# Performance work log

Measured on AMD Instinct MI355X. Metric: run time of the kernel, lower is better.

## Reference

```python
import jax, jax.numpy as jnp
import numpy as np

EMBED_DIM = 1024
ATTN_DIM = 1024
BATCH = 4
SEQ = 2048


def setup_inputs() -> dict:
    key = jax.random.key(0)
    k1, k2, k3, k4 = jax.random.split(key, 4)
    embedded = jax.random.normal(k1, (BATCH, SEQ, EMBED_DIM), dtype=jnp.float32)
    # torch Linear weights have shape [out_features, in_features]
    scale = 1.0 / np.sqrt(EMBED_DIM)
    W_K = jax.random.uniform(k2, (ATTN_DIM, EMBED_DIM), dtype=jnp.float32, minval=-scale, maxval=scale)
    W_Q = jax.random.uniform(k3, (ATTN_DIM, EMBED_DIM), dtype=jnp.float32, minval=-scale, maxval=scale)
    W_V = jax.random.uniform(k4, (ATTN_DIM, EMBED_DIM), dtype=jnp.float32, minval=-scale, maxval=scale)
    return {"embedded": embedded, "W_K": W_K, "W_Q": W_Q, "W_V": W_V}


def reference(embedded, W_K, W_Q, W_V):
    # embedded: [B, L, E]; W_*: [A, E] (torch Linear layout, applied as x @ W.T)
    L = embedded.shape[1]
    A = W_K.shape[0]
    K = jnp.einsum('ble,ae->bla', embedded, W_K)
    Q = jnp.einsum('ble,ae->bla', embedded, W_Q)
    V = jnp.einsum('ble,ae->bla', embedded, W_V)
    att = jnp.einsum('bqa,bka->bqk', Q, K) / jnp.sqrt(jnp.float32(A))  # [B, L, L]
    causal = jnp.tril(jnp.ones((L, L), dtype=bool))  # lower-triangular mask
    att = jnp.where(causal, att, -jnp.inf)
    att = jax.nn.softmax(att, axis=-1)
    return jnp.einsum('bqk,bka->bqa', att, V)
```

## Files before the change

kernel.cpp:

```cpp
#include <hip/hip_runtime.h>
#include <hip/hip_bf16.h>
#include <stdint.h>

#define BATCH 4
#define SEQ   2048
#define EMB   1024
#define ADIM  1024

typedef __attribute__((ext_vector_type(8))) short  short8;
typedef __attribute__((ext_vector_type(4))) float  float4v;

static __device__ __forceinline__ unsigned short f2bf(float f) {
    unsigned int u = __float_as_uint(f);
    u += 0x7FFFu + ((u >> 16) & 1u);
    return (unsigned short)(u >> 16);
}

static __device__ __forceinline__ uint2 pack4(float4v v) {
    uint2 r;
    r.x = (unsigned)f2bf(v.x) | ((unsigned)f2bf(v.y) << 16);
    r.y = (unsigned)f2bf(v.z) | ((unsigned)f2bf(v.w) << 16);
    return r;
}

static __device__ __forceinline__ void gload16(const void* g, void* l) {
    __builtin_amdgcn_global_load_lds(
        (const __attribute__((address_space(1))) void*)g,
        (__attribute__((address_space(3))) void*)l, 16, 0, 0);
}

__global__ __launch_bounds__(256) void prep_kernel(
    const float* __restrict__ X,  const float* __restrict__ Wv,
    const float* __restrict__ Wq, const float* __restrict__ Wk,
    unsigned short* __restrict__ Xb, unsigned short* __restrict__ Wvb,
    unsigned short* __restrict__ WqT, unsigned short* __restrict__ WkT,
    float* __restrict__ rowsum)
{
    __shared__ unsigned short T[64][72];
    const int bI = blockIdx.x;
    if (bI < 4608) {
        const float* src; unsigned short* dst; int off;
        if (bI < 4096) { src = X;  dst = Xb;  off = bI; }
        else           { src = Wv; dst = Wvb; off = bI - 4096; }
        const int i = (off * 256 + threadIdx.x) * 8;
        float4v a = *(const float4v*)(src + i);
        float4v b = *(const float4v*)(src + i + 4);
        uint2 pa = pack4(a), pb = pack4(b);
        uint4 o; o.x = pa.x; o.y = pa.y; o.z = pb.x; o.w = pb.y;
        *(uint4*)(dst + i) = o;
        return;
    }
    if (bI < 4616) {
        const int i = ((bI - 4616) * 256 + threadIdx.x) * 4;
        *(float4v*)(rowsum + i) = float4v{0.f, 0.f, 0.f, 0.f};
        return;
    }
    const int z    = (bI - 4616) >> 8;
    const int tile = (bI - 4616) & 255;
    const int ti = tile >> 4;
    const int tj = tile & 15;
    const float* W = z ? Wk : Wq;
    unsigned short* WT = z ? WkT : WqT;
    const int t  = threadIdx.x;
    const int r  = t >> 2;
    const int c  = (t & 3) << 4;

    const float* src = W + (size_t)(ti * 64 + r) * EMB + tj * 64 + c;
    #pragma unroll
    for (int u = 0; u < 4; ++u) {
        float4v v = *(const float4v*)(src + 4 * u);
        uint2 p = pack4(v);
        *(uint2*)&T[r][c + 4 * u] = p;
    }
    __syncthreads();
    unsigned short tmp[16];
    #pragma unroll
    for (int u = 0; u < 16; ++u) tmp[u] = T[c + u][r];
    unsigned short* dst = WT + (size_t)(tj * 64 + r) * EMB + ti * 64 + c;
    *(uint4*)(dst)     = *(uint4*)&tmp[0];
    *(uint4*)(dst + 8) = *(uint4*)&tmp[8];
}

static __device__ __forceinline__ void gemm_core(
    const unsigned short* __restrict__ A, const unsigned short* __restrict__ B,
    int lda, int ldb, int m0, int n0, int kend,
    unsigned short* As, unsigned short* Bs, float4v acc[4][4])
{
    const int tid  = threadIdx.x;
    const int r    = tid >> 2;
    const int c8   = (tid & 3) << 3;
    const int lane = tid & 63;
    const int wave = tid >> 6;
    const int quad = lane >> 4;
    const int l16  = lane & 15;
    const int wm   = (wave >> 1) << 6;
    const int wn   = (wave & 1) << 6;

    const unsigned short* Ag = A + (size_t)(m0 + r) * lda + c8;
    const unsigned short* Bg = B + (size_t)(n0 + r) * ldb + c8;
    unsigned short* Al = As + tid * 8;
    unsigned short* Bl = Bs + tid * 8;
    const int niter = kend >> 5;

    #define ISSUE(k0, st) do { \
        unsigned short* al_ = Al + (st) * 4096; \
        unsigned short* bl_ = Bl + (st) * 4096; \
        gload16(Ag + (k0),                    al_); \
        gload16(Ag + (k0) + (size_t)64 * lda, al_ + 2048); \
        gload16(Bg + (k0),                    bl_); \
        gload16(Bg + (k0) + (size_t)64 * ldb, bl_ + 2048); \
    } while (0)

    ISSUE(0, 0);
    ISSUE(32, 1);

    int ci = 0, ii = 2;
    for (int it = 0; it < niter; ++it) {
        const int knext = (it + 2 < niter) ? ((it + 2) << 5) : 0;
        ISSUE(knext, ii);
        asm volatile("s_waitcnt vmcnt(8)" ::: "memory");
        asm volatile("s_barrier" ::: "memory");

        const unsigned short* Ah = As + ci * 4096;
        const unsigned short* Bh = Bs + ci * 4096;
        short8 af[4], bfr[4];
        #pragma unroll
        for (int i = 0; i < 4; ++i)
            af[i] = *(const short8*)&Ah[(wm + 16 * i + l16) * 32 + quad * 8];
        #pragma unroll
        for (int j = 0; j < 4; ++j)
            bfr[j] = *(const short8*)&Bh[(wn + 16 * j + l16) * 32 + quad * 8];
        #pragma unroll
        for (int i = 0; i < 4; ++i)
            #pragma unroll
            for (int j = 0; j < 4; ++j)
                acc[i][j] = __builtin_amdgcn_mfma_f32_16x16x32_bf16(af[i], bfr[j], acc[i][j], 0, 0, 0);

        asm volatile("s_barrier" ::: "memory");
        ci = (ci == 2) ? 0 : ci + 1;
        ii = (ii == 2) ? 0 : ii + 1;
    }
    asm volatile("s_waitcnt vmcnt(0)" ::: "memory");
    #undef ISSUE
}

#define DECL_TILE_IDX() \
    const int lane = threadIdx.x & 63; \
    const int wave = threadIdx.x >> 6; \
    const int quad = lane >> 4; \
    const int l16  = lane & 15; \
    const int wm   = (wave >> 1) << 6; \
    const int wn   = (wave & 1) << 6;

__global__ __launch_bounds__(256, 3) void m_kernel(
    const unsigned short* __restrict__ WkT, const unsigned short* __restrict__ WqT,
    unsigned short* __restrict__ Mt)
{
    __shared__ __align__(16) unsigned short As[3 * 128 * 32];
    __shared__ __align__(16) unsigned short Bs[3 * 128 * 32];
    const int m0 = (blockIdx.x >> 3) << 7;
    const int n0 = (blockIdx.x & 7) << 7;

    float4v acc[4][4];
    #pragma unroll
    for (int i = 0; i < 4; ++i)
        #pragma unroll
        for (int j = 0; j < 4; ++j)
            acc[i][j] = float4v{0.f, 0.f, 0.f, 0.f};

    gemm_core(WkT, WqT, EMB, EMB, m0, n0, EMB, As, Bs, acc);

    DECL_TILE_IDX();
    const float scale = 0.03125f;
    #pragma unroll
    for (int i = 0; i < 4; ++i)
        #pragma unroll
        for (int j = 0; j < 4; ++j)
            #pragma unroll
            for (int rr = 0; rr < 4; ++rr) {
                const int row = m0 + wm + 16 * i + quad * 4 + rr;
                const int col = n0 + wn + 16 * j + l16;
                Mt[(size_t)row * EMB + col] = f2bf(acc[i][j][rr] * scale);
            }
}

__global__ __launch_bounds__(256, 2) void qv_kernel(
    const unsigned short* __restrict__ Xb, const unsigned short* __restrict__ Mt,
    const unsigned short* __restrict__ Wvb,
    unsigned short* __restrict__ Qpb, unsigned short* __restrict__ Vtb)
{
    __shared__ __align__(16) unsigned short LDS[3 * 4096 + 3 * 8192];
    unsigned short* As = LDS;
    unsigned short* Bs = LDS + 3 * 4096;
    const int idx   = blockIdx.x;
    const int mlow  = idx & 7;
    const int n0    = ((idx >> 3) & 3) << 8;
    const int mhigh = (idx >> 5) & 7;
    const int z     = idx >> 8;
    const int m0    = ((mhigh << 3) | mlow) << 7;
    const unsigned short* B = (z == 0) ? Mt : Wvb;

    const int tid  = threadIdx.x;
    const int r    = tid >> 2;
    const int c8   = (tid & 3) << 3;
    const int lane = tid & 63;
    const int wave = tid >> 6;
    const int quad = lane >> 4;
    const int l16  = lane & 15;
    const int wm   = (wave >> 1) << 6;
    const int wn   = (wave & 1) << 7;

    float4v acc[4][8];
    #pragma unroll
    for (int i = 0; i < 4; ++i)
        #pragma unroll
        for (int j = 0; j < 8; ++j)
            acc[i][j] = float4v{0.f, 0.f, 0.f, 0.f};

    const unsigned short* Ag = Xb + (size_t)(m0 + r) * EMB + c8;
    const unsigned short* Bg = B  + (size_t)(n0 + r) * EMB + c8;
    unsigned short* Al = As + tid * 8;
    unsigned short* Bl = Bs + tid * 8;

    #define ISSUE_W(k0, st) do { \
        unsigned short* al_ = Al + (st) * 4096; \
        unsigned short* bl_ = Bl + (st) * 8192; \
        gload16(Ag + (k0),                     al_); \
        gload16(Ag + (k0) + (size_t)64  * EMB, al_ + 2048); \
        gload16(Bg + (k0),                     bl_); \
        gload16(Bg + (k0) + (size_t)64  * EMB, bl_ + 2048); \
        gload16(Bg + (k0) + (size_t)128 * EMB, bl_ + 4096); \
        gload16(Bg + (k0) + (size_t)192 * EMB, bl_ + 6144); \
    } while (0)

    ISSUE_W(0, 0);
    ISSUE_W(32, 1);

    int ci = 0, ii = 2;
    for (int it = 0; it < 32; ++it) {
        const int knext = (it + 2 < 32) ? ((it + 2) << 5) : 0;
        ISSUE_W(knext, ii);
        asm volatile("s_waitcnt vmcnt(12)" ::: "memory");
        asm volatile("s_barrier" ::: "memory");

        const unsigned short* Ah = As + ci * 4096;
        const unsigned short* Bh = Bs + ci * 8192;
        short8 af[4], bfr[8];
        #pragma unroll
        for (int i = 0; i < 4; ++i)
            af[i] = *(const short8*)&Ah[(wm + 16 * i + l16) * 32 + quad * 8];
        #pragma unroll
        for (int j = 0; j < 8; ++j)
            bfr[j] = *(const short8*)&Bh[(wn + 16 * j + l16) * 32 + quad * 8];
        #pragma unroll
        for (int i = 0; i < 4; ++i)
            #pragma unroll
            for (int j = 0; j < 8; ++j)
                acc[i][j] = __builtin_amdgcn_mfma_f32_16x16x32_bf16(af[i], bfr[j], acc[i][j], 0, 0, 0);

        asm volatile("s_barrier" ::: "memory");
        ci = (ci == 2) ? 0 : ci + 1;
        ii = (ii == 2) ? 0 : ii + 1;
    }
    asm volatile("s_waitcnt vmcnt(0)" ::: "memory");
    #undef ISSUE_W

    if (z == 0) {
        #pragma unroll
        for (int i = 0; i < 4; ++i)
            #pragma unroll
            for (int j = 0; j < 8; ++j)
                #pragma unroll
                for (int rr = 0; rr < 4; ++rr) {
                    const int row = m0 + wm + 16 * i + quad * 4 + rr;
                    const int col = n0 + wn + 16 * j + l16;
                    Qpb[(size_t)row * ADIM + col] = f2bf(acc[i][j][rr]);
                }
    } else {
        __syncthreads();
        unsigned short* T = LDS;
        #pragma unroll
        for (int i = 0; i < 4; ++i)
            #pragma unroll
            for (int j = 0; j < 8; ++j) {
                const int qrow = wm + 16 * i + quad * 4;
                const int acol = wn + 16 * j + l16;
                uint2 w;
                w.x = (unsigned)f2bf(acc[i][j][0]) | ((unsigned)f2bf(acc[i][j][1]) << 16);
                w.y = (unsigned)f2bf(acc[i][j][2]) | ((unsigned)f2bf(acc[i][j][3]) << 16);
                *(uint2*)&T[acol * 136 + qrow] = w;
            }
        __syncthreads();
        const int bb = m0 >> 11;
        const int l0 = m0 & (SEQ - 1);
        unsigned short* dst = Vtb + (((size_t)(bb * ADIM + n0 + tid)) << 11) + l0;
        #pragma unroll
        for (int u = 0; u < 16; ++u)
            *(uint4*)(dst + u * 8) = *(const uint4*)&T[tid * 136 + u * 8];
    }
}

__global__ __launch_bounds__(256, 3) void s_kernel(
    const unsigned short* __restrict__ Qpb, const unsigned short* __restrict__ Xb,
    unsigned short* __restrict__ E, float* __restrict__ rowsum)
{
    const int idx = blockIdx.x;
    const int b   = idx & 3;
    const int tri = idx >> 2;
    int qt = 0;
    while (((qt + 1) * (qt + 2)) / 2 <= tri) ++qt;
    const int kt = tri - (qt * (qt + 1)) / 2;
    const int q0 = qt << 7;
    const int k0 = kt << 7;

    __shared__ __align__(16) unsigned short As[3 * 128 * 32];
    __shared__ __align__(16) unsigned short Bs[3 * 128 * 32];

    float4v acc[4][4];
    #pragma unroll
    for (int i = 0; i < 4; ++i)
        #pragma unroll
        for (int j = 0; j < 4; ++j)
            acc[i][j] = float4v{0.f, 0.f, 0.f, 0.f};

    gemm_core(Qpb + (size_t)b * SEQ * ADIM, Xb + (size_t)b * SEQ * EMB,
              ADIM, EMB, q0, k0, EMB, As, Bs, acc);

    unsigned short* Eb = E + (size_t)b * SEQ * SEQ;
    float* rsb = rowsum + (size_t)b * SEQ;
    DECL_TILE_IDX();
    #pragma unroll
    for (int i = 0; i < 4; ++i)
        #pragma unroll
        for (int rr = 0; rr < 4; ++rr) {
            const int row = q0 + wm + 16 * i + quad * 4 + rr;
            float s = 0.f;
            #pragma unroll
            for (int j = 0; j < 4; ++j) {
                const int col = k0 + wn + 16 * j + l16;
                float e = (col <= row) ? __expf(acc[i][j][rr]) : 0.f;
                s += e;
                Eb[(size_t)row * SEQ + col] = f2bf(e);
            }
            s += __shfl_xor(s, 1);
            s += __shfl_xor(s, 2);
            s += __shfl_xor(s, 4);
            s += __shfl_xor(s, 8);
            if (l16 == 0) atomicAdd(&rsb[row], s);
        }
}

__global__ __launch_bounds__(256, 3) void pv_kernel(
    const unsigned short* __restrict__ E, const unsigned short* __restrict__ Vtb,
    const float* __restrict__ rowsum, float* __restrict__ out)
{
    const int idx = blockIdx.x;
    const int t   = (idx < 256) ? (15 - (idx >> 5)) : ((idx - 256) >> 5);
    const int rem = idx & 31;
    const int b   = rem >> 3;
    const int a0  = (rem & 7) << 7;
    const int q0  = t << 7;

    __shared__ __align__(16) unsigned short As[3 * 128 * 32];
    __shared__ __align__(16) unsigned short Bs[3 * 128 * 32];

    float4v acc[4][4];
    #pragma unroll
    for (int i = 0; i < 4; ++i)
        #pragma unroll
        for (int j = 0; j < 4; ++j)
            acc[i][j] = float4v{0.f, 0.f, 0.f, 0.f};

    gemm_core(E + (size_t)b * SEQ * SEQ, Vtb + (size_t)b * ADIM * SEQ,
              SEQ, SEQ, q0, a0, q0 + 128, As, Bs, acc);

    float* ob = out + (size_t)b * SEQ * ADIM;
    const float* rsb = rowsum + (size_t)b * SEQ;
    DECL_TILE_IDX();
    #pragma unroll
    for (int i = 0; i < 4; ++i)
        #pragma unroll
        for (int rr = 0; rr < 4; ++rr) {
            const int row = q0 + wm + 16 * i + quad * 4 + rr;
            const float inv = 1.0f / rsb[row];
            #pragma unroll
            for (int j = 0; j < 4; ++j) {
                const int col = a0 + wn + 16 * j + l16;
                ob[(size_t)row * ADIM + col] = acc[i][j][rr] * inv;
            }
        }
}

extern "C" void kernel_launch(void* const* d_in, const int* in_sizes, int n_in,
                              void* d_out, int out_size, void* d_ws, size_t ws_size,
                              hipStream_t stream)
{
    const float* X  = (const float*)d_in[0];
    const float* Wk = (const float*)d_in[1];
    const float* Wq = (const float*)d_in[2];
    const float* Wv = (const float*)d_in[3];
    float* out = (float*)d_out;

    const size_t MB = 1024 * 1024;
    char* ws = (char*)d_ws;
    unsigned short* Xb  = (unsigned short*)(ws);
    unsigned short* Wvb = (unsigned short*)(ws + 16 * MB);
    unsigned short* WqT = (unsigned short*)(ws + 18 * MB);
    unsigned short* WkT = (unsigned short*)(ws + 20 * MB);
    unsigned short* Mt  = (unsigned short*)(ws + 22 * MB);
    unsigned short* Qpb = (unsigned short*)(ws + 24 * MB);
    unsigned short* E   = (unsigned short*)(ws + 40 * MB);
    unsigned short* Vtb = (unsigned short*)(ws + 72 * MB);
    float*          rowsum = (float*)(ws + 88 * MB);

    hipLaunchKernelGGL(prep_kernel, dim3(5128), dim3(256), 0, stream,
                       X, Wv, Wq, Wk, Xb, Wvb, WqT, WkT, rowsum);
    hipLaunchKernelGGL(m_kernel, dim3(64), dim3(256), 0, stream, WkT, WqT, Mt);
    hipLaunchKernelGGL(qv_kernel, dim3(512), dim3(256), 0, stream,
                       Xb, Mt, Wvb, Qpb, Vtb);
    hipLaunchKernelGGL(s_kernel, dim3(4 * 136), dim3(256), 0, stream, Qpb, Xb, E, rowsum);
    hipLaunchKernelGGL(pv_kernel, dim3(512), dim3(256), 0, stream, E, Vtb, rowsum, out);
}
```

Measured before the change: 228.2 us.

## Deepen GEMM pipeline to four stages and retile qv kernel to 128x128

The shared GEMM core moves from a three-stage to a four-stage LDS prefetch ring with a wait count adjusted to match. Occupancy hints drop from three to two blocks per CU to make room for the larger LDS. The qv kernel stops using its own 128x256 loop and calls the shared 128x128 gemm_core over twice as many blocks, with a reworked V-transpose store. The rowsum zeroing index, which was negative before and wrote out of bounds, is also corrected. The aim is more memory-latency hiding and better load balance, at the cost of lower occupancy and more reloads of the A tile.

```diff
diff --git a/kernel.cpp b/kernel.cpp
--- a/kernel.cpp
+++ b/kernel.cpp
@@ -51,7 +51,7 @@
         return;
     }
     if (bI < 4616) {
-        const int i = ((bI - 4616) * 256 + threadIdx.x) * 4;
+        const int i = ((bI - 4608) * 256 + threadIdx.x) * 4;
         *(float4v*)(rowsum + i) = float4v{0.f, 0.f, 0.f, 0.f};
         return;
     }
@@ -113,12 +113,13 @@
 
     ISSUE(0, 0);
     ISSUE(32, 1);
-
-    int ci = 0, ii = 2;
+    ISSUE(64, 2);
+
+    int ci = 0, ii = 3;
     for (int it = 0; it < niter; ++it) {
-        const int knext = (it + 2 < niter) ? ((it + 2) << 5) : 0;
+        const int knext = (it + 3 < niter) ? ((it + 3) << 5) : 0;
         ISSUE(knext, ii);
-        asm volatile("s_waitcnt vmcnt(8)" ::: "memory");
+        asm volatile("s_waitcnt vmcnt(12)" ::: "memory");
         asm volatile("s_barrier" ::: "memory");
 
         const unsigned short* Ah = As + ci * 4096;
@@ -137,8 +138,8 @@
                 acc[i][j] = __builtin_amdgcn_mfma_f32_16x16x32_bf16(af[i], bfr[j], acc[i][j], 0, 0, 0);
 
         asm volatile("s_barrier" ::: "memory");
-        ci = (ci == 2) ? 0 : ci + 1;
-        ii = (ii == 2) ? 0 : ii + 1;
+        ci = (ci + 1) & 3;
+        ii = (ii + 1) & 3;
     }
     asm volatile("s_waitcnt vmcnt(0)" ::: "memory");
     #undef ISSUE
@@ -152,12 +153,12 @@
     const int wm   = (wave >> 1) << 6; \
     const int wn   = (wave & 1) << 6;
 
-__global__ __launch_bounds__(256, 3) void m_kernel(
+__global__ __launch_bounds__(256, 2) void m_kernel(
     const unsigned short* __restrict__ WkT, const unsigned short* __restrict__ WqT,
     unsigned short* __restrict__ Mt)
 {
-    __shared__ __align__(16) unsigned short As[3 * 128 * 32];
-    __shared__ __align__(16) unsigned short Bs[3 * 128 * 32];
+    __shared__ __align__(16) unsigned short As[4 * 128 * 32];
+    __shared__ __align__(16) unsigned short Bs[4 * 128 * 32];
     const int m0 = (blockIdx.x >> 3) << 7;
     const int n0 = (blockIdx.x & 7) << 7;
 
@@ -189,87 +190,32 @@
     const unsigned short* __restrict__ Wvb,
     unsigned short* __restrict__ Qpb, unsigned short* __restrict__ Vtb)
 {
-    __shared__ __align__(16) unsigned short LDS[3 * 4096 + 3 * 8192];
+    __shared__ __align__(16) unsigned short LDS[2 * 4 * 128 * 32];
     unsigned short* As = LDS;
-    unsigned short* Bs = LDS + 3 * 4096;
+    unsigned short* Bs = LDS + 4 * 128 * 32;
     const int idx   = blockIdx.x;
     const int mlow  = idx & 7;
-    const int n0    = ((idx >> 3) & 3) << 8;
-    const int mhigh = (idx >> 5) & 7;
-    const int z     = idx >> 8;
+    const int n0    = ((idx >> 3) & 7) << 7;
+    const int mhigh = (idx >> 6) & 7;
+    const int z     = idx >> 9;
     const int m0    = ((mhigh << 3) | mlow) << 7;
     const unsigned short* B = (z == 0) ? Mt : Wvb;
 
-    const int tid  = threadIdx.x;
-    const int r    = tid >> 2;
-    const int c8   = (tid & 3) << 3;
-    const int lane = tid & 63;
-    const int wave = tid >> 6;
-    const int quad = lane >> 4;
-    const int l16  = lane & 15;
-    const int wm   = (wave >> 1) << 6;
-    const int wn   = (wave & 1) << 7;
-
-    float4v acc[4][8];
-    #pragma unroll
-    for (int i = 0; i < 4; ++i)
-        #pragma unroll
-        for (int j = 0; j < 8; ++j)
+    float4v acc[4][4];
+    #pragma unroll
+    for (int i = 0; i < 4; ++i)
+        #pragma unroll
+        for (int j = 0; j < 4; ++j)
             acc[i][j] = float4v{0.f, 0.f, 0.f, 0.f};
 
-    const unsigned short* Ag = Xb + (size_t)(m0 + r) * EMB + c8;
-    const unsigned short* Bg = B  + (size_t)(n0 + r) * EMB + c8;
-    unsigned short* Al = As + tid * 8;
-    unsigned short* Bl = Bs + tid * 8;
-
-    #define ISSUE_W(k0, st) do { \
-        unsigned short* al_ = Al + (st) * 4096; \
-        unsigned short* bl_ = Bl + (st) * 8192; \
-        gload16(Ag + (k0),                     al_); \
-        gload16(Ag + (k0) + (size_t)64  * EMB, al_ + 2048); \
-        gload16(Bg + (k0),                     bl_); \
-        gload16(Bg + (k0) + (size_t)64  * EMB, bl_ + 2048); \
-        gload16(Bg + (k0) + (size_t)128 * EMB, bl_ + 4096); \
-        gload16(Bg + (k0) + (size_t)192 * EMB, bl_ + 6144); \
-    } while (0)
-
-    ISSUE_W(0, 0);
-    ISSUE_W(32, 1);
-
-    int ci = 0, ii = 2;
-    for (int it = 0; it < 32; ++it) {
-        const int knext = (it + 2 < 32) ? ((it + 2) << 5) : 0;
-        ISSUE_W(knext, ii);
-        asm volatile("s_waitcnt vmcnt(12)" ::: "memory");
-        asm volatile("s_barrier" ::: "memory");
-
-        const unsigned short* Ah = As + ci * 4096;
-        const unsigned short* Bh = Bs + ci * 8192;
-        short8 af[4], bfr[8];
+    gemm_core(Xb, B, EMB, EMB, m0, n0, EMB, As, Bs, acc);
+
+    DECL_TILE_IDX();
+    if (z == 0) {
         #pragma unroll
         for (int i = 0; i < 4; ++i)
-            af[i] = *(const short8*)&Ah[(wm + 16 * i + l16) * 32 + quad * 8];
-        #pragma unroll
-        for (int j = 0; j < 8; ++j)
-            bfr[j] = *(const short8*)&Bh[(wn + 16 * j + l16) * 32 + quad * 8];
-        #pragma unroll
-        for (int i = 0; i < 4; ++i)
-            #pragma unroll
-            for (int j = 0; j < 8; ++j)
-                acc[i][j] = __builtin_amdgcn_mfma_f32_16x16x32_bf16(af[i], bfr[j], acc[i][j], 0, 0, 0);
-
-        asm volatile("s_barrier" ::: "memory");
-        ci = (ci == 2) ? 0 : ci + 1;
-        ii = (ii == 2) ? 0 : ii + 1;
-    }
-    asm volatile("s_waitcnt vmcnt(0)" ::: "memory");
-    #undef ISSUE_W
-
-    if (z == 0) {
-        #pragma unroll
-        for (int i = 0; i < 4; ++i)
-            #pragma unroll
-            for (int j = 0; j < 8; ++j)
+            #pragma unroll
+            for (int j = 0; j < 4; ++j)
                 #pragma unroll
                 for (int rr = 0; rr < 4; ++rr) {
                     const int row = m0 + wm + 16 * i + quad * 4 + rr;
@@ -282,7 +228,7 @@
         #pragma unroll
         for (int i = 0; i < 4; ++i)
             #pragma unroll
-            for (int j = 0; j < 8; ++j) {
+            for (int j = 0; j < 4; ++j) {
                 const int qrow = wm + 16 * i + quad * 4;
                 const int acol = wn + 16 * j + l16;
                 uint2 w;
@@ -291,16 +237,19 @@
                 *(uint2*)&T[acol * 136 + qrow] = w;
             }
         __syncthreads();
-        const int bb = m0 >> 11;
-        const int l0 = m0 & (SEQ - 1);
-        unsigned short* dst = Vtb + (((size_t)(bb * ADIM + n0 + tid)) << 11) + l0;
-        #pragma unroll
-        for (int u = 0; u < 16; ++u)
-            *(uint4*)(dst + u * 8) = *(const uint4*)&T[tid * 136 + u * 8];
-    }
-}
-
-__global__ __launch_bounds__(256, 3) void s_kernel(
+        const int tid = threadIdx.x;
+        const int bb  = m0 >> 11;
+        const int l0  = m0 & (SEQ - 1);
+        const int acol = tid >> 1;
+        const int qh   = (tid & 1) << 6;
+        unsigned short* dst = Vtb + (((size_t)(bb * ADIM + n0 + acol)) << 11) + l0 + qh;
+        #pragma unroll
+        for (int u = 0; u < 8; ++u)
+            *(uint4*)(dst + u * 8) = *(const uint4*)&T[acol * 136 + qh + u * 8];
+    }
+}
+
+__global__ __launch_bounds__(256, 2) void s_kernel(
     const unsigned short* __restrict__ Qpb, const unsigned short* __restrict__ Xb,
     unsigned short* __restrict__ E, float* __restrict__ rowsum)
 {
@@ -313,8 +262,8 @@
     const int q0 = qt << 7;
     const int k0 = kt << 7;
 
-    __shared__ __align__(16) unsigned short As[3 * 128 * 32];
-    __shared__ __align__(16) unsigned short Bs[3 * 128 * 32];
+    __shared__ __align__(16) unsigned short As[4 * 128 * 32];
+    __shared__ __align__(16) unsigned short Bs[4 * 128 * 32];
 
     float4v acc[4][4];
     #pragma unroll
@@ -350,7 +299,7 @@
         }
 }
 
-__global__ __launch_bounds__(256, 3) void pv_kernel(
+__global__ __launch_bounds__(256, 2) void pv_kernel(
     const unsigned short* __restrict__ E, const unsigned short* __restrict__ Vtb,
     const float* __restrict__ rowsum, float* __restrict__ out)
 {
@@ -361,8 +310,8 @@
     const int a0  = (rem & 7) << 7;
     const int q0  = t << 7;
 
-    __shared__ __align__(16) unsigned short As[3 * 128 * 32];
-    __shared__ __align__(16) unsigned short Bs[3 * 128 * 32];
+    __shared__ __align__(16) unsigned short As[4 * 128 * 32];
+    __shared__ __align__(16) unsigned short Bs[4 * 128 * 32];
 
     float4v acc[4][4];
     #pragma unroll
@@ -416,7 +365,7 @@
     hipLaunchKernelGGL(prep_kernel, dim3(5128), dim3(256), 0, stream,
                        X, Wv, Wq, Wk, Xb, Wvb, WqT, WkT, rowsum);
     hipLaunchKernelGGL(m_kernel, dim3(64), dim3(256), 0, stream, WkT, WqT, Mt);
-    hipLaunchKernelGGL(qv_kernel, dim3(512), dim3(256), 0, stream,
+    hipLaunchKernelGGL(qv_kernel, dim3(1024), dim3(256), 0, stream,
                        Xb, Mt, Wvb, Qpb, Vtb);
     hipLaunchKernelGGL(s_kernel, dim3(4 * 136), dim3(256), 0, stream, Qpb, Xb, E, rowsum);
     hipLaunchKernelGGL(pv_kernel, dim3(512), dim3(256), 0, stream, E, Vtb, rowsum, out);
```

After: 246.1 us. 1.08x slower.

## Enlarge qv_kernel tiles to 256x256 and fix rowsum zeroing index

Applied to the files above, without the earlier changes.

The fused Q/V projection GEMM moves from 128x256 to 256x256 output tiles per block. Each wave now holds an 8x8 grid of MFMA accumulators, the grid halves to 256 blocks, and a swizzled block index groups blocks by M tile. This raises arithmetic intensity per LDS and global load and cuts total global traffic, at the cost of one block per CU, heavy register use, and the V transpose now running in two LDS passes. It also fixes the rowsum zeroing offset, which previously computed a negative index and did not clear the buffer.

```diff
diff --git a/kernel.cpp b/kernel.cpp
--- a/kernel.cpp
+++ b/kernel.cpp
@@ -51,7 +51,7 @@
         return;
     }
     if (bI < 4616) {
-        const int i = ((bI - 4616) * 256 + threadIdx.x) * 4;
+        const int i = ((bI - 4608) * 256 + threadIdx.x) * 4;
         *(float4v*)(rowsum + i) = float4v{0.f, 0.f, 0.f, 0.f};
         return;
     }
@@ -184,21 +184,23 @@
             }
 }
 
-__global__ __launch_bounds__(256, 2) void qv_kernel(
+__global__ __launch_bounds__(256, 1) void qv_kernel(
     const unsigned short* __restrict__ Xb, const unsigned short* __restrict__ Mt,
     const unsigned short* __restrict__ Wvb,
     unsigned short* __restrict__ Qpb, unsigned short* __restrict__ Vtb)
 {
-    __shared__ __align__(16) unsigned short LDS[3 * 4096 + 3 * 8192];
+    __shared__ __align__(16) unsigned short LDS[49152];
     unsigned short* As = LDS;
-    unsigned short* Bs = LDS + 3 * 4096;
-    const int idx   = blockIdx.x;
-    const int mlow  = idx & 7;
-    const int n0    = ((idx >> 3) & 3) << 8;
-    const int mhigh = (idx >> 5) & 7;
-    const int z     = idx >> 8;
-    const int m0    = ((mhigh << 3) | mlow) << 7;
-    const unsigned short* B = (z == 0) ? Mt : Wvb;
+    unsigned short* Bs = LDS + 24576;
+
+    const int idx  = blockIdx.x;
+    const int swz  = (idx & 7) * 32 + (idx >> 3);
+    const int mt   = swz >> 3;
+    const int slot = swz & 7;
+    const int z    = slot >> 2;
+    const int n0   = (slot & 3) << 8;
+    const int m0   = mt << 8;
+    const unsigned short* B = z ? Wvb : Mt;
 
     const int tid  = threadIdx.x;
     const int r    = tid >> 2;
@@ -207,12 +209,12 @@
     const int wave = tid >> 6;
     const int quad = lane >> 4;
     const int l16  = lane & 15;
-    const int wm   = (wave >> 1) << 6;
+    const int wm   = (wave >> 1) << 7;
     const int wn   = (wave & 1) << 7;
 
-    float4v acc[4][8];
-    #pragma unroll
-    for (int i = 0; i < 4; ++i)
+    float4v acc[8][8];
+    #pragma unroll
+    for (int i = 0; i < 8; ++i)
         #pragma unroll
         for (int j = 0; j < 8; ++j)
             acc[i][j] = float4v{0.f, 0.f, 0.f, 0.f};
@@ -222,38 +224,40 @@
     unsigned short* Al = As + tid * 8;
     unsigned short* Bl = Bs + tid * 8;
 
-    #define ISSUE_W(k0, st) do { \
-        unsigned short* al_ = Al + (st) * 4096; \
+    #define ISSUE_Q(k0, st) do { \
+        unsigned short* al_ = Al + (st) * 8192; \
         unsigned short* bl_ = Bl + (st) * 8192; \
         gload16(Ag + (k0),                     al_); \
         gload16(Ag + (k0) + (size_t)64  * EMB, al_ + 2048); \
+        gload16(Ag + (k0) + (size_t)128 * EMB, al_ + 4096); \
+        gload16(Ag + (k0) + (size_t)192 * EMB, al_ + 6144); \
         gload16(Bg + (k0),                     bl_); \
         gload16(Bg + (k0) + (size_t)64  * EMB, bl_ + 2048); \
         gload16(Bg + (k0) + (size_t)128 * EMB, bl_ + 4096); \
         gload16(Bg + (k0) + (size_t)192 * EMB, bl_ + 6144); \
     } while (0)
 
-    ISSUE_W(0, 0);
-    ISSUE_W(32, 1);
+    ISSUE_Q(0, 0);
+    ISSUE_Q(32, 1);
 
     int ci = 0, ii = 2;
     for (int it = 0; it < 32; ++it) {
         const int knext = (it + 2 < 32) ? ((it + 2) << 5) : 0;
-        ISSUE_W(knext, ii);
-        asm volatile("s_waitcnt vmcnt(12)" ::: "memory");
+        ISSUE_Q(knext, ii);
+        asm volatile("s_waitcnt vmcnt(16)" ::: "memory");
         asm volatile("s_barrier" ::: "memory");
 
-        const unsigned short* Ah = As + ci * 4096;
+        const unsigned short* Ah = As + ci * 8192;
         const unsigned short* Bh = Bs + ci * 8192;
-        short8 af[4], bfr[8];
-        #pragma unroll
-        for (int i = 0; i < 4; ++i)
+        short8 af[8], bfr[8];
+        #pragma unroll
+        for (int i = 0; i < 8; ++i)
             af[i] = *(const short8*)&Ah[(wm + 16 * i + l16) * 32 + quad * 8];
         #pragma unroll
         for (int j = 0; j < 8; ++j)
             bfr[j] = *(const short8*)&Bh[(wn + 16 * j + l16) * 32 + quad * 8];
         #pragma unroll
-        for (int i = 0; i < 4; ++i)
+        for (int i = 0; i < 8; ++i)
             #pragma unroll
             for (int j = 0; j < 8; ++j)
                 acc[i][j] = __builtin_amdgcn_mfma_f32_16x16x32_bf16(af[i], bfr[j], acc[i][j], 0, 0, 0);
@@ -263,11 +267,11 @@
         ii = (ii == 2) ? 0 : ii + 1;
     }
     asm volatile("s_waitcnt vmcnt(0)" ::: "memory");
-    #undef ISSUE_W
+    #undef ISSUE_Q
 
     if (z == 0) {
         #pragma unroll
-        for (int i = 0; i < 4; ++i)
+        for (int i = 0; i < 8; ++i)
             #pragma unroll
             for (int j = 0; j < 8; ++j)
                 #pragma unroll
@@ -277,26 +281,30 @@
                     Qpb[(size_t)row * ADIM + col] = f2bf(acc[i][j][rr]);
                 }
     } else {
-        __syncthreads();
-        unsigned short* T = LDS;
-        #pragma unroll
-        for (int i = 0; i < 4; ++i)
-            #pragma unroll
-            for (int j = 0; j < 8; ++j) {
-                const int qrow = wm + 16 * i + quad * 4;
-                const int acol = wn + 16 * j + l16;
-                uint2 w;
-                w.x = (unsigned)f2bf(acc[i][j][0]) | ((unsigned)f2bf(acc[i][j][1]) << 16);
-                w.y = (unsigned)f2bf(acc[i][j][2]) | ((unsigned)f2bf(acc[i][j][3]) << 16);
-                *(uint2*)&T[acol * 136 + qrow] = w;
-            }
-        __syncthreads();
         const int bb = m0 >> 11;
         const int l0 = m0 & (SEQ - 1);
-        unsigned short* dst = Vtb + (((size_t)(bb * ADIM + n0 + tid)) << 11) + l0;
-        #pragma unroll
-        for (int u = 0; u < 16; ++u)
-            *(uint4*)(dst + u * 8) = *(const uint4*)&T[tid * 136 + u * 8];
+        #pragma unroll
+        for (int h = 0; h < 2; ++h) {
+            __syncthreads();
+            if ((wm >> 7) == h) {
+                #pragma unroll
+                for (int i = 0; i < 8; ++i)
+                    #pragma unroll
+                    for (int j = 0; j < 8; ++j) {
+                        const int qrow = 16 * i + quad * 4;
+                        const int acol = wn + 16 * j + l16;
+                        uint2 w;
+                        w.x = (unsigned)f2bf(acc[i][j][0]) | ((unsigned)f2bf(acc[i][j][1]) << 16);
+                        w.y = (unsigned)f2bf(acc[i][j][2]) | ((unsigned)f2bf(acc[i][j][3]) << 16);
+                        *(uint2*)&LDS[acol * 136 + qrow] = w;
+                    }
+            }
+            __syncthreads();
+            unsigned short* dst = Vtb + (((size_t)(bb * ADIM + n0 + tid)) << 11) + l0 + h * 128;
+            #pragma unroll
+            for (int u = 0; u < 16; ++u)
+                *(uint4*)(dst + u * 8) = *(const uint4*)&LDS[tid * 136 + u * 8];
+        }
     }
 }
 
@@ -416,7 +424,7 @@
     hipLaunchKernelGGL(prep_kernel, dim3(5128), dim3(256), 0, stream,
                        X, Wv, Wq, Wk, Xb, Wvb, WqT, WkT, rowsum);
     hipLaunchKernelGGL(m_kernel, dim3(64), dim3(256), 0, stream, WkT, WqT, Mt);
-    hipLaunchKernelGGL(qv_kernel, dim3(512), dim3(256), 0, stream,
+    hipLaunchKernelGGL(qv_kernel, dim3(256), dim3(256), 0, stream,
                        Xb, Mt, Wvb, Qpb, Vtb);
     hipLaunchKernelGGL(s_kernel, dim3(4 * 136), dim3(256), 0, stream, Qpb, Xb, E, rowsum);
     hipLaunchKernelGGL(pv_kernel, dim3(512), dim3(256), 0, stream, E, Vtb, rowsum, out);
```

New measurement: 240.9 us. 5.6% more time.

## Split-K the weight product and load-balance causal tiles with paired scheduling

Applied to the files above, without the earlier changes.

The M = Wk^T·Wq GEMM is split four ways along K into fp32 partials, which a new reduce kernel sums and converts to bf16, so 256 blocks run instead of 64. The PV kernel splits long causal rows into two K-halves that accumulate into a pre-zeroed output with atomics. The S and QV kernels are re-indexed to pair short and long q-tiles per group for better balance. It also fixes the rowsum zeroing offset. Costs include an extra launch, fp32 partial traffic, atomics on the output, and zeroing half the output in prep.

```diff
diff --git a/kernel.cpp b/kernel.cpp
--- a/kernel.cpp
+++ b/kernel.cpp
@@ -34,7 +34,7 @@
     const float* __restrict__ Wq, const float* __restrict__ Wk,
     unsigned short* __restrict__ Xb, unsigned short* __restrict__ Wvb,
     unsigned short* __restrict__ WqT, unsigned short* __restrict__ WkT,
-    float* __restrict__ rowsum)
+    float* __restrict__ rowsum, float* __restrict__ out)
 {
     __shared__ unsigned short T[64][72];
     const int bI = blockIdx.x;
@@ -51,8 +51,17 @@
         return;
     }
     if (bI < 4616) {
-        const int i = ((bI - 4616) * 256 + threadIdx.x) * 4;
+        const int i = ((bI - 4608) * 256 + threadIdx.x) * 4;
         *(float4v*)(rowsum + i) = float4v{0.f, 0.f, 0.f, 0.f};
+        return;
+    }
+    if (bI >= 5128) {
+        const int o   = bI - 5128;
+        const int b   = o >> 10;
+        const int blk = o & 1023;
+        float* dst = out + ((size_t)(b * 2048 + 1024) * 1024)
+                         + (size_t)blk * 1024 + threadIdx.x * 4;
+        *(float4v*)dst = float4v{0.f, 0.f, 0.f, 0.f};
         return;
     }
     const int z    = (bI - 4616) >> 8;
@@ -83,7 +92,7 @@
 
 static __device__ __forceinline__ void gemm_core(
     const unsigned short* __restrict__ A, const unsigned short* __restrict__ B,
-    int lda, int ldb, int m0, int n0, int kend,
+    int lda, int ldb, int m0, int n0, int klen,
     unsigned short* As, unsigned short* Bs, float4v acc[4][4])
 {
     const int tid  = threadIdx.x;
@@ -100,7 +109,7 @@
     const unsigned short* Bg = B + (size_t)(n0 + r) * ldb + c8;
     unsigned short* Al = As + tid * 8;
     unsigned short* Bl = Bs + tid * 8;
-    const int niter = kend >> 5;
+    const int niter = klen >> 5;
 
     #define ISSUE(k0, st) do { \
         unsigned short* al_ = Al + (st) * 4096; \
@@ -154,12 +163,15 @@
 
 __global__ __launch_bounds__(256, 3) void m_kernel(
     const unsigned short* __restrict__ WkT, const unsigned short* __restrict__ WqT,
-    unsigned short* __restrict__ Mt)
+    float* __restrict__ Mtf)
 {
     __shared__ __align__(16) unsigned short As[3 * 128 * 32];
     __shared__ __align__(16) unsigned short Bs[3 * 128 * 32];
-    const int m0 = (blockIdx.x >> 3) << 7;
-    const int n0 = (blockIdx.x & 7) << 7;
+    const int idx = blockIdx.x;
+    const int kc  = idx >> 6;
+    const int t   = idx & 63;
+    const int m0  = (t >> 3) << 7;
+    const int n0  = (t & 7) << 7;
 
     float4v acc[4][4];
     #pragma unroll
@@ -168,10 +180,10 @@
         for (int j = 0; j < 4; ++j)
             acc[i][j] = float4v{0.f, 0.f, 0.f, 0.f};
 
-    gemm_core(WkT, WqT, EMB, EMB, m0, n0, EMB, As, Bs, acc);
-
+    gemm_core(WkT + kc * 256, WqT + kc * 256, EMB, EMB, m0, n0, 256, As, Bs, acc);
+
+    float* dst = Mtf + (size_t)kc * 1024 * 1024;
     DECL_TILE_IDX();
-    const float scale = 0.03125f;
     #pragma unroll
     for (int i = 0; i < 4; ++i)
         #pragma unroll
@@ -180,8 +192,25 @@
             for (int rr = 0; rr < 4; ++rr) {
                 const int row = m0 + wm + 16 * i + quad * 4 + rr;
                 const int col = n0 + wn + 16 * j + l16;
-                Mt[(size_t)row * EMB + col] = f2bf(acc[i][j][rr] * scale);
+                dst[(size_t)row * EMB + col] = acc[i][j][rr];
             }
+}
+
+__global__ __launch_bounds__(256) void mc_kernel(
+    const float* __restrict__ Mtf, unsigned short* __restrict__ Mt)
+{
+    const int base = (blockIdx.x * 256 + threadIdx.x) * 16;
+    #pragma unroll
+    for (int u = 0; u < 4; ++u) {
+        const int i = base + u * 4;
+        float4v s = *(const float4v*)(Mtf + i);
+        s = s + *(const float4v*)(Mtf + 1048576 + i);
+        s = s + *(const float4v*)(Mtf + 2097152 + i);
+        s = s + *(const float4v*)(Mtf + 3145728 + i);
+        s = s * 0.03125f;
+        uint2 p = pack4(s);
+        *(uint2*)(Mt + i) = p;
+    }
 }
 
 __global__ __launch_bounds__(256, 2) void qv_kernel(
@@ -192,12 +221,16 @@
     __shared__ __align__(16) unsigned short LDS[3 * 4096 + 3 * 8192];
     unsigned short* As = LDS;
     unsigned short* Bs = LDS + 3 * 4096;
-    const int idx   = blockIdx.x;
-    const int mlow  = idx & 7;
-    const int n0    = ((idx >> 3) & 3) << 8;
-    const int mhigh = (idx >> 5) & 7;
-    const int z     = idx >> 8;
-    const int m0    = ((mhigh << 3) | mlow) << 7;
+    const int idx = blockIdx.x;
+    const int x   = idx & 7;
+    const int j   = idx >> 3;
+    const int sl  = j & 7;
+    const int g   = j >> 3;
+    const int z   = sl >> 2;
+    const int n0  = (sl & 3) << 8;
+    const int b   = g & 3;
+    const int qt  = (g >> 2) ? (15 - x) : x;
+    const int m0  = (b * 16 + qt) << 7;
     const unsigned short* B = (z == 0) ? Mt : Wvb;
 
     const int tid  = threadIdx.x;
@@ -214,8 +247,8 @@
     #pragma unroll
     for (int i = 0; i < 4; ++i)
         #pragma unroll
-        for (int j = 0; j < 8; ++j)
-            acc[i][j] = float4v{0.f, 0.f, 0.f, 0.f};
+        for (int jj = 0; jj < 8; ++jj)
+            acc[i][jj] = float4v{0.f, 0.f, 0.f, 0.f};
 
     const unsigned short* Ag = Xb + (size_t)(m0 + r) * EMB + c8;
     const unsigned short* Bg = B  + (size_t)(n0 + r) * EMB + c8;
@@ -250,13 +283,13 @@
         for (int i = 0; i < 4; ++i)
             af[i] = *(const short8*)&Ah[(wm + 16 * i + l16) * 32 + quad * 8];
         #pragma unroll
-        for (int j = 0; j < 8; ++j)
-            bfr[j] = *(const short8*)&Bh[(wn + 16 * j + l16) * 32 + quad * 8];
-        #pragma unroll
-        for (int i = 0; i < 4; ++i)
-            #pragma unroll
-            for (int j = 0; j < 8; ++j)
-                acc[i][j] = __builtin_amdgcn_mfma_f32_16x16x32_bf16(af[i], bfr[j], acc[i][j], 0, 0, 0);
+        for (int jj = 0; jj < 8; ++jj)
+            bfr[jj] = *(const short8*)&Bh[(wn + 16 * jj + l16) * 32 + quad * 8];
+        #pragma unroll
+        for (int i = 0; i < 4; ++i)
+            #pragma unroll
+            for (int jj = 0; jj < 8; ++jj)
+                acc[i][jj] = __builtin_amdgcn_mfma_f32_16x16x32_bf16(af[i], bfr[jj], acc[i][jj], 0, 0, 0);
 
         asm volatile("s_barrier" ::: "memory");
         ci = (ci == 2) ? 0 : ci + 1;
@@ -269,12 +302,12 @@
         #pragma unroll
         for (int i = 0; i < 4; ++i)
             #pragma unroll
-            for (int j = 0; j < 8; ++j)
+            for (int jj = 0; jj < 8; ++jj)
                 #pragma unroll
                 for (int rr = 0; rr < 4; ++rr) {
                     const int row = m0 + wm + 16 * i + quad * 4 + rr;
-                    const int col = n0 + wn + 16 * j + l16;
-                    Qpb[(size_t)row * ADIM + col] = f2bf(acc[i][j][rr]);
+                    const int col = n0 + wn + 16 * jj + l16;
+                    Qpb[(size_t)row * ADIM + col] = f2bf(acc[i][jj][rr]);
                 }
     } else {
         __syncthreads();
@@ -282,12 +315,12 @@
         #pragma unroll
         for (int i = 0; i < 4; ++i)
             #pragma unroll
-            for (int j = 0; j < 8; ++j) {
+            for (int jj = 0; jj < 8; ++jj) {
                 const int qrow = wm + 16 * i + quad * 4;
-                const int acol = wn + 16 * j + l16;
+                const int acol = wn + 16 * jj + l16;
                 uint2 w;
-                w.x = (unsigned)f2bf(acc[i][j][0]) | ((unsigned)f2bf(acc[i][j][1]) << 16);
-                w.y = (unsigned)f2bf(acc[i][j][2]) | ((unsigned)f2bf(acc[i][j][3]) << 16);
+                w.x = (unsigned)f2bf(acc[i][jj][0]) | ((unsigned)f2bf(acc[i][jj][1]) << 16);
+                w.y = (unsigned)f2bf(acc[i][jj][2]) | ((unsigned)f2bf(acc[i][jj][3]) << 16);
                 *(uint2*)&T[acol * 136 + qrow] = w;
             }
         __syncthreads();
@@ -305,13 +338,14 @@
     unsigned short* __restrict__ E, float* __restrict__ rowsum)
 {
     const int idx = blockIdx.x;
-    const int b   = idx & 3;
-    const int tri = idx >> 2;
-    int qt = 0;
-    while (((qt + 1) * (qt + 2)) / 2 <= tri) ++qt;
-    const int kt = tri - (qt * (qt + 1)) / 2;
-    const int q0 = qt << 7;
-    const int k0 = kt << 7;
+    const int x   = idx & 7;
+    const int j   = idx >> 3;
+    const int b   = j / 17;
+    const int u   = j - b * 17;
+    const int qt  = (u <= x) ? x : 15 - x;
+    const int kt  = (u <= x) ? u : u - (x + 1);
+    const int q0  = qt << 7;
+    const int k0  = kt << 7;
 
     __shared__ __align__(16) unsigned short As[3 * 128 * 32];
     __shared__ __align__(16) unsigned short Bs[3 * 128 * 32];
@@ -320,8 +354,8 @@
     #pragma unroll
     for (int i = 0; i < 4; ++i)
         #pragma unroll
-        for (int j = 0; j < 4; ++j)
-            acc[i][j] = float4v{0.f, 0.f, 0.f, 0.f};
+        for (int jj = 0; jj < 4; ++jj)
+            acc[i][jj] = float4v{0.f, 0.f, 0.f, 0.f};
 
     gemm_core(Qpb + (size_t)b * SEQ * ADIM, Xb + (size_t)b * SEQ * EMB,
               ADIM, EMB, q0, k0, EMB, As, Bs, acc);
@@ -336,9 +370,9 @@
             const int row = q0 + wm + 16 * i + quad * 4 + rr;
             float s = 0.f;
             #pragma unroll
-            for (int j = 0; j < 4; ++j) {
-                const int col = k0 + wn + 16 * j + l16;
-                float e = (col <= row) ? __expf(acc[i][j][rr]) : 0.f;
+            for (int jj = 0; jj < 4; ++jj) {
+                const int col = k0 + wn + 16 * jj + l16;
+                float e = (col <= row) ? __expf(acc[i][jj][rr]) : 0.f;
                 s += e;
                 Eb[(size_t)row * SEQ + col] = f2bf(e);
             }
@@ -354,12 +388,19 @@
     const unsigned short* __restrict__ E, const unsigned short* __restrict__ Vtb,
     const float* __restrict__ rowsum, float* __restrict__ out)
 {
-    const int idx = blockIdx.x;
-    const int t   = (idx < 256) ? (15 - (idx >> 5)) : ((idx - 256) >> 5);
-    const int rem = idx & 31;
-    const int b   = rem >> 3;
-    const int a0  = (rem & 7) << 7;
-    const int q0  = t << 7;
+    const int idx  = blockIdx.x;
+    const int x    = idx & 7;
+    const int j    = idx >> 3;
+    const int slot = j >> 5;
+    const int c    = j & 31;
+    const int b    = c >> 3;
+    const int a0   = (c & 7) << 7;
+
+    int qt, kbeg, klen, dual;
+    if (slot == 0)      { qt = x;      kbeg = 0;    klen = (x + 1) << 7; dual = 0; }
+    else if (slot == 1) { qt = 15 - x; kbeg = 0;    klen = 1024;         dual = 1; }
+    else                { qt = 15 - x; kbeg = 1024; klen = (8 - x) << 7; dual = 1; }
+    const int q0 = qt << 7;
 
     __shared__ __align__(16) unsigned short As[3 * 128 * 32];
     __shared__ __align__(16) unsigned short Bs[3 * 128 * 32];
@@ -368,27 +409,42 @@
     #pragma unroll
     for (int i = 0; i < 4; ++i)
         #pragma unroll
-        for (int j = 0; j < 4; ++j)
-            acc[i][j] = float4v{0.f, 0.f, 0.f, 0.f};
-
-    gemm_core(E + (size_t)b * SEQ * SEQ, Vtb + (size_t)b * ADIM * SEQ,
-              SEQ, SEQ, q0, a0, q0 + 128, As, Bs, acc);
+        for (int jj = 0; jj < 4; ++jj)
+            acc[i][jj] = float4v{0.f, 0.f, 0.f, 0.f};
+
+    gemm_core(E + (size_t)b * SEQ * SEQ + kbeg, Vtb + (size_t)b * ADIM * SEQ + kbeg,
+              SEQ, SEQ, q0, a0, klen, As, Bs, acc);
 
     float* ob = out + (size_t)b * SEQ * ADIM;
     const float* rsb = rowsum + (size_t)b * SEQ;
     DECL_TILE_IDX();
-    #pragma unroll
-    for (int i = 0; i < 4; ++i)
-        #pragma unroll
-        for (int rr = 0; rr < 4; ++rr) {
-            const int row = q0 + wm + 16 * i + quad * 4 + rr;
-            const float inv = 1.0f / rsb[row];
-            #pragma unroll
-            for (int j = 0; j < 4; ++j) {
-                const int col = a0 + wn + 16 * j + l16;
-                ob[(size_t)row * ADIM + col] = acc[i][j][rr] * inv;
+    if (!dual) {
+        #pragma unroll
+        for (int i = 0; i < 4; ++i)
+            #pragma unroll
+            for (int rr = 0; rr < 4; ++rr) {
+                const int row = q0 + wm + 16 * i + quad * 4 + rr;
+                const float inv = 1.0f / rsb[row];
+                #pragma unroll
+                for (int jj = 0; jj < 4; ++jj) {
+                    const int col = a0 + wn + 16 * jj + l16;
+                    ob[(size_t)row * ADIM + col] = acc[i][jj][rr] * inv;
+                }
             }
-        }
+    } else {
+        #pragma unroll
+        for (int i = 0; i < 4; ++i)
+            #pragma unroll
+            for (int rr = 0; rr < 4; ++rr) {
+                const int row = q0 + wm + 16 * i + quad * 4 + rr;
+                const float inv = 1.0f / rsb[row];
+                #pragma unroll
+                for (int jj = 0; jj < 4; ++jj) {
+                    const int col = a0 + wn + 16 * jj + l16;
+                    atomicAdd(&ob[(size_t)row * ADIM + col], acc[i][jj][rr] * inv);
+                }
+            }
+    }
 }
 
 extern "C" void kernel_launch(void* const* d_in, const int* in_sizes, int n_in,
@@ -412,12 +468,14 @@
     unsigned short* E   = (unsigned short*)(ws + 40 * MB);
     unsigned short* Vtb = (unsigned short*)(ws + 72 * MB);
     float*          rowsum = (float*)(ws + 88 * MB);
-
-    hipLaunchKernelGGL(prep_kernel, dim3(5128), dim3(256), 0, stream,
-                       X, Wv, Wq, Wk, Xb, Wvb, WqT, WkT, rowsum);
-    hipLaunchKernelGGL(m_kernel, dim3(64), dim3(256), 0, stream, WkT, WqT, Mt);
+    float*          Mtf = (float*)(ws + 40 * MB);
+
+    hipLaunchKernelGGL(prep_kernel, dim3(9224), dim3(256), 0, stream,
+                       X, Wv, Wq, Wk, Xb, Wvb, WqT, WkT, rowsum, out);
+    hipLaunchKernelGGL(m_kernel, dim3(256), dim3(256), 0, stream, WkT, WqT, Mtf);
+    hipLaunchKernelGGL(mc_kernel, dim3(256), dim3(256), 0, stream, Mtf, Mt);
     hipLaunchKernelGGL(qv_kernel, dim3(512), dim3(256), 0, stream,
                        Xb, Mt, Wvb, Qpb, Vtb);
-    hipLaunchKernelGGL(s_kernel, dim3(4 * 136), dim3(256), 0, stream, Qpb, Xb, E, rowsum);
-    hipLaunchKernelGGL(pv_kernel, dim3(512), dim3(256), 0, stream, E, Vtb, rowsum, out);
-}
+    hipLaunchKernelGGL(s_kernel, dim3(544), dim3(256), 0, stream, Qpb, Xb, E, rowsum);
+    hipLaunchKernelGGL(pv_kernel, dim3(768), dim3(256), 0, stream, E, Vtb, rowsum, out);
+}
```

Measured after the change: 230.0 us. No clear change (+0.8%).
